# Optimization experiments

Measured on AMD Instinct MI355X. Metric: run time of the kernel, lower is better.

Reference implementation:

```python
import jax, jax.numpy as jnp
import numpy as np

N, D, B = 50000, 256, 2048
SIGMA = 1.0
SIGMA2 = SIGMA * SIGMA  # module stores np.square(sigma)


def setup_inputs() -> dict:
    key = jax.random.key(0)
    k1, k2, k3, k4 = jax.random.split(key, 4)
    x = jax.random.normal(k1, (B, D), dtype=jnp.float32)
    data_set = jax.random.normal(k2, (N, D), dtype=jnp.float32)
    # labels are +/-1
    data_labels = jnp.where(jax.random.uniform(k3, (N,)) < 0.5, -1.0, 1.0).astype(jnp.float32)
    # lambdas initialized to ones in the module; use small positive noise around 1/n scale
    lambdas = jax.random.uniform(k4, (N,), dtype=jnp.float32) * (2.0 / N)
    b = jnp.ones((1,), dtype=jnp.float32)
    return {"x": x, "data_set": data_set, "data_labels": data_labels,
            "lambdas": lambdas, "b": b}


def reference(x, data_set, data_labels, lambdas, b):
    x2 = jnp.sum(x * x, axis=1, keepdims=True)            # [B,1]
    s2 = jnp.sum(data_set * data_set, axis=1)             # [N]
    cross = jnp.einsum('bd,nd->bn', x, data_set)          # [B,N]
    sqdist = x2 + s2[None, :] - 2.0 * cross               # [B,N]
    K = jnp.exp(-sqdist / (2.0 * SIGMA2))                 # rbf kernel [B,N]
    w = data_labels * jax.nn.relu(lambdas)                # [N]
    return jnp.tanh(K @ w + b)                            # [B]
```

## Files before the change

kernel.cpp:

```cpp
#include <hip/hip_runtime.h>
#include <hip/hip_bf16.h>
#include <hip/hip_fp8.h>
#include <math.h>

#define NPTS 50000
#define DIM  256
#define BQ   2048
#define NPAD 50048

#define CH   32
#define NCH32 1564
#define NG   96
#define LOG2E 1.4426950408889634f

#define WS_ACC 0
#define WS_X2  2048
#define WS_T   4096
#define WS_SGN 54144
#define WS_XB  104192
#define WS_SB  366336
#define WS_TOTAL_BYTES (6772480ull * 4ull)

#define V1_ACC 0
#define V1_X2  2048
#define V1_S2  4096
#define V1_W   54096

typedef __bf16 bf16x8 __attribute__((ext_vector_type(8)));
typedef __bf16 bf16x4 __attribute__((ext_vector_type(4)));
typedef float  f32x4  __attribute__((ext_vector_type(4)));
typedef float  f32x16 __attribute__((ext_vector_type(16)));
typedef int    i32x4  __attribute__((ext_vector_type(4)));
typedef int    i32x8  __attribute__((ext_vector_type(8)));
typedef unsigned int u32;
typedef unsigned char u8;

__device__ __forceinline__ float fast_exp2(float v) {
#if __has_builtin(__builtin_amdgcn_exp2f)
  return __builtin_amdgcn_exp2f(v);
#else
  return exp2f(v);
#endif
}

__device__ __forceinline__ float fast_log2(float v) {
#if __has_builtin(__builtin_amdgcn_logf)
  return __builtin_amdgcn_logf(v);
#else
  return __log2f(v);
#endif
}

__device__ __forceinline__ void async_copy16(const void* g, void* l) {
  __builtin_amdgcn_global_load_lds(
      (const __attribute__((address_space(1))) u32*)g,
      (__attribute__((address_space(3))) u32*)l, 16, 0, 0);
}

__device__ __forceinline__ u32 pack_fp8x4(float4 v) {
#if __has_builtin(__builtin_amdgcn_cvt_pk_fp8_f32)
  int pk = __builtin_amdgcn_cvt_pk_fp8_f32(v.x, v.y, 0, false);
  pk = __builtin_amdgcn_cvt_pk_fp8_f32(v.z, v.w, pk, true);
  return (u32)pk;
#else
  __hip_fp8_e4m3 a(v.x), b(v.y), c(v.z), d(v.w);
  return (u32)a.__x | ((u32)b.__x << 8) | ((u32)c.__x << 16) | ((u32)d.__x << 24);
#endif
}


__global__ __launch_bounds__(256) void svm_precvt10(
    const float* __restrict__ x, const float* __restrict__ s,
    const float* __restrict__ labels, const float* __restrict__ lambdas,
    float* __restrict__ ws) {
  const int wid  = blockIdx.x * 4 + (threadIdx.x >> 6);
  const int lane = threadIdx.x & 63;
  u8* xb8 = (u8*)(ws + WS_XB);
  u8* sb8 = (u8*)(ws + WS_SB);

  if (blockIdx.x < 8) ws[WS_ACC + blockIdx.x * 256 + threadIdx.x] = 0.0f;

  if (wid < NPAD) {
    float4 v = make_float4(0.f, 0.f, 0.f, 0.f);
    if (wid < NPTS)
      v = reinterpret_cast<const float4*>(s + (size_t)wid * DIM)[lane];
    ((u32*)(sb8 + (size_t)wid * DIM))[lane] = pack_fp8x4(v);
    float ss = v.x * v.x + v.y * v.y + v.z * v.z + v.w * v.w;
    #pragma unroll
    for (int off = 32; off > 0; off >>= 1) ss += __shfl_xor(ss, off);
    if (lane == 0) {
      float s2h = 0.5f * LOG2E * ss;
      float lam = (wid < NPTS) ? lambdas[wid] : 0.0f;
      float lab = (wid < NPTS) ? labels[wid] : 1.0f;
      float mag = lam > 0.0f ? lam : 0.0f;
      ws[WS_T + wid]   = (mag > 0.0f) ? s2h - fast_log2(mag) : __builtin_inff();
      ws[WS_SGN + wid] = lab;
    }
  } else if (wid < NPAD + BQ) {
    int r = wid - NPAD;
    float4 v = reinterpret_cast<const float4*>(x + (size_t)r * DIM)[lane];
    ((u32*)(xb8 + (size_t)r * DIM))[lane] = pack_fp8x4(v);
    float ss = v.x * v.x + v.y * v.y + v.z * v.z + v.w * v.w;
    #pragma unroll
    for (int off = 32; off > 0; off >>= 1) ss += __shfl_xor(ss, off);
    if (lane == 0) ws[WS_X2 + r] = 0.5f * LOG2E * ss;
  }
}

__global__ __launch_bounds__(256, 2) void svm_main21(float* __restrict__ ws) {
  __shared__ u8 sB[3][8192];

  const u8* xb8 = (const u8*)(ws + WS_XB);
  const u8* sb8 = (const u8*)(ws + WS_SB);
  const float* x2g = ws + WS_X2;
  const float* tg  = ws + WS_T;
  const float* sgg = ws + WS_SGN;
  float* accOut    = ws + WS_ACC;

  const int t    = threadIdx.x;
  const int wave = t >> 6;
  const int lane = t & 63;
  const int l32  = lane & 31;
  const int hk   = lane >> 5;
  const int g    = blockIdx.x % NG;
  const int mt   = blockIdx.x / NG;
  const int m0   = mt * 256;
  const int c0   = (NCH32 * g) / NG;
  const int c1   = (NCH32 * (g + 1)) / NG;

#define STAGE21(buf, cc)                                                      \
  do {                                                                        \
    _Pragma("unroll")                                                         \
    for (int i = 0; i < 2; ++i) {                                             \
      int p  = wave * 2 + i;                                        \
      int kt = p >> 1;                                              \
      int h  = p & 1;                                                         \
      int r  = h * 16 + (lane >> 2);                                          \
      int q  = (lane & 3) ^ ((r >> 1) & 3);                                   \
      const u8* src = sb8 + (size_t)((cc) * CH + r) * DIM + kt * 64 + q * 16; \
      async_copy16(src, &sB[(buf)][kt * 2048 + h * 1024 + lane * 16]);        \
    }                                                                         \
  } while (0)

  STAGE21(0, c0);
  STAGE21(1, c0 + 1);

  i32x8 afr[2][4];
  #pragma unroll
  for (int mi = 0; mi < 2; ++mi)
    #pragma unroll
    for (int kt = 0; kt < 4; ++kt) {
      const u8* ap = xb8 + (size_t)(m0 + wave * 64 + mi * 32 + l32) * DIM
                         + kt * 64 + hk * 32;
      i32x4 a0 = *reinterpret_cast<const i32x4*>(ap);
      i32x4 a1 = *reinterpret_cast<const i32x4*>(ap + 16);
      afr[mi][kt] = __builtin_shufflevector(a0, a1, 0, 1, 2, 3, 4, 5, 6, 7);
    }
  #pragma unroll
  for (int mi = 0; mi < 2; ++mi)
    #pragma unroll
    for (int kt = 0; kt < 4; ++kt)
      asm volatile("" : "+v"(afr[mi][kt]));

  float runAcc0[16], runAcc1[16];
  #pragma unroll
  for (int i = 0; i < 16; ++i) { runAcc0[i] = 0.0f; runAcc1[i] = 0.0f; }

  asm volatile("s_waitcnt vmcnt(2)" ::: "memory");
  __builtin_amdgcn_s_barrier();

  int cur = 0;
  for (int c = c0; c < c1; ++c) {
    float tt = tg[c * CH + l32];
    float sg = sgg[c * CH + l32];
    __builtin_amdgcn_sched_barrier(0);

    {
      int c2 = c + 2;
      if (c2 < c1) {
        int b2 = cur + 2; if (b2 >= 3) b2 -= 3;
        STAGE21(b2, c2);
      }
    }

    f32x16 acc0 = (f32x16)(0.0f), acc1 = (f32x16)(0.0f);
    const u8* bufB = &sB[cur][0];
    __builtin_amdgcn_s_setprio(1);
    #pragma unroll
    for (int kt = 0; kt < 4; ++kt) {
      int s0 = ((l32 << 2) | (hk << 1)) ^ ((l32 >> 1) & 3);
      const u8* bp = bufB + kt * 2048;
      i32x4 lo = *reinterpret_cast<const i32x4*>(bp + s0 * 16);
      i32x4 hi = *reinterpret_cast<const i32x4*>(bp + (s0 ^ 1) * 16);
      i32x8 bfr = __builtin_shufflevector(lo, hi, 0, 1, 2, 3, 4, 5, 6, 7);
      acc0 = __builtin_amdgcn_mfma_scale_f32_32x32x64_f8f6f4(
          afr[0][kt], bfr, acc0, 0, 0, 0, 0x7F7F7F7F, 0, 0x7F7F7F7F);
      acc1 = __builtin_amdgcn_mfma_scale_f32_32x32x64_f8f6f4(
          afr[1][kt], bfr, acc1, 0, 0, 0, 0x7F7F7F7F, 0, 0x7F7F7F7F);
    }
    __builtin_amdgcn_s_setprio(0);

    #pragma unroll
    for (int reg = 0; reg < 16; ++reg)
      runAcc0[reg] = __builtin_fmaf(
          sg, fast_exp2(__builtin_fmaf(acc0[reg], LOG2E, -tt)), runAcc0[reg]);
    #pragma unroll
    for (int reg = 0; reg < 16; ++reg)
      runAcc1[reg] = __builtin_fmaf(
          sg, fast_exp2(__builtin_fmaf(acc1[reg], LOG2E, -tt)), runAcc1[reg]);

    __builtin_amdgcn_s_barrier();
    asm volatile("" ::: "memory");
    cur = (cur + 1 < 3) ? cur + 1 : 0;
  }

  #pragma unroll
  for (int reg = 0; reg < 16; ++reg) {
    float v = runAcc0[reg];
    v += __shfl_xor(v, 1);
    v += __shfl_xor(v, 2);
    v += __shfl_xor(v, 4);
    v += __shfl_xor(v, 8);
    v += __shfl_xor(v, 16);
    if (l32 == 0) {
      int row = m0 + wave * 64 + (reg & 3) + 8 * (reg >> 2) + 4 * hk;
      atomicAdd(&accOut[row], fast_exp2(-x2g[row]) * v);
    }
  }
  #pragma unroll
  for (int reg = 0; reg < 16; ++reg) {
    float v = runAcc1[reg];
    v += __shfl_xor(v, 1);
    v += __shfl_xor(v, 2);
    v += __shfl_xor(v, 4);
    v += __shfl_xor(v, 8);
    v += __shfl_xor(v, 16);
    if (l32 == 0) {
      int row = m0 + wave * 64 + 32 + (reg & 3) + 8 * (reg >> 2) + 4 * hk;
      atomicAdd(&accOut[row], fast_exp2(-x2g[row]) * v);
    }
  }
#undef STAGE21
}


#define BK 32

__global__ __launch_bounds__(256) void svm_precompute(
    const float* __restrict__ x, const float* __restrict__ s,
    const float* __restrict__ labels, const float* __restrict__ lambdas,
    float* __restrict__ ws) {
  int wid  = blockIdx.x * 4 + (threadIdx.x >> 6);
  int lane = threadIdx.x & 63;
  const float* src;
  if (wid < NPTS)           src = s + (size_t)wid * DIM;
  else if (wid < NPTS + BQ) src = x + (size_t)(wid - NPTS) * DIM;
  else return;
  float4 v = reinterpret_cast<const float4*>(src)[lane];
  float ss = v.x * v.x + v.y * v.y + v.z * v.z + v.w * v.w;
  #pragma unroll
  for (int off = 32; off > 0; off >>= 1) ss += __shfl_xor(ss, off);
  if (lane == 0) {
    if (wid < NPTS) {
      ws[V1_S2 + wid] = ss;
      float lam = lambdas[wid];
      ws[V1_W + wid] = labels[wid] * (lam > 0.0f ? lam : 0.0f);
    } else {
      ws[V1_X2 + (wid - NPTS)] = ss;
    }
  }
}

__global__ __launch_bounds__(256) void svm_main(
    const float* __restrict__ x, const float* __restrict__ s,
    const float* __restrict__ ws) {
  __shared__ __bf16 sA[128 * BK];
  __shared__ __bf16 sB2[128 * BK];

  const int t    = threadIdx.x;
  const int wave = t >> 6;
  const int lane = t & 63;
  const int quad = lane >> 4;
  const int l16  = lane & 15;
  const int wm   = (wave & 1) * 64;
  const int wn   = (wave >> 1) * 64;
  const int bRow0 = blockIdx.y * 128;
  const int n0    = blockIdx.x * 128;

  f32x4 acc[4][4];
  #pragma unroll
  for (int i = 0; i < 4; ++i)
    #pragma unroll
    for (int j = 0; j < 4; ++j)
      acc[i][j] = (f32x4)(0.0f);

  for (int kt = 0; kt < DIM / BK; ++kt) {
    const int k0 = kt * BK;
    __syncthreads();
    #pragma unroll
    for (int i = 0; i < 4; ++i) {
      int slot = t + i * 256;
      int r  = slot >> 3;
      int c4 = slot & 7;
      float4 va = reinterpret_cast<const float4*>(
          x + (size_t)(bRow0 + r) * DIM + k0)[c4];
      bf16x4 ha = { (__bf16)va.x, (__bf16)va.y, (__bf16)va.z, (__bf16)va.w };
      *reinterpret_cast<bf16x4*>(&sA[r * BK + c4 * 4]) = ha;

      int nrow = n0 + r;
      float4 vb = make_float4(0.f, 0.f, 0.f, 0.f);
      if (nrow < NPTS)
        vb = reinterpret_cast<const float4*>(
            s + (size_t)nrow * DIM + k0)[c4];
      bf16x4 hb = { (__bf16)vb.x, (__bf16)vb.y, (__bf16)vb.z, (__bf16)vb.w };
      *reinterpret_cast<bf16x4*>(&sB2[r * BK + c4 * 4]) = hb;
    }
    __syncthreads();

    bf16x8 af[4], bfv[4];
    #pragma unroll
    for (int mi = 0; mi < 4; ++mi)
      af[mi] = *reinterpret_cast<const bf16x8*>(
          &sA[(wm + mi * 16 + l16) * BK + quad * 8]);
    #pragma unroll
    for (int ni = 0; ni < 4; ++ni)
      bfv[ni] = *reinterpret_cast<const bf16x8*>(
          &sB2[(wn + ni * 16 + l16) * BK + quad * 8]);
    #pragma unroll
    for (int mi = 0; mi < 4; ++mi)
      #pragma unroll
      for (int ni = 0; ni < 4; ++ni)
        acc[mi][ni] = __builtin_amdgcn_mfma_f32_16x16x32_bf16(
            af[mi], bfv[ni], acc[mi][ni], 0, 0, 0);
  }

  const float* x2g = ws + V1_X2;
  const float* s2g = ws + V1_S2;
  const float* wg  = ws + V1_W;
  float* accOut    = (float*)ws + V1_ACC;

  float s2v[4], wv[4];
  #pragma unroll
  for (int ni = 0; ni < 4; ++ni) {
    int n = n0 + wn + ni * 16 + l16;
    bool ok = n < NPTS;
    s2v[ni] = ok ? s2g[n] : 0.0f;
    wv[ni]  = ok ? wg[n]  : 0.0f;
  }
  #pragma unroll
  for (int mi = 0; mi < 4; ++mi) {
    const int mbase = wm + mi * 16 + quad * 4;
    #pragma unroll
    for (int reg = 0; reg < 4; ++reg) {
      float x2r = x2g[bRow0 + mbase + reg];
      float ps = 0.0f;
      #pragma unroll
      for (int ni = 0; ni < 4; ++ni) {
        float cc = acc[mi][ni][reg];
        ps += __expf(__builtin_fmaf(-0.5f, x2r + s2v[ni], cc)) * wv[ni];
      }
      ps += __shfl_xor(ps, 1);
      ps += __shfl_xor(ps, 2);
      ps += __shfl_xor(ps, 4);
      ps += __shfl_xor(ps, 8);
      if (l16 == 0) atomicAdd(&accOut[bRow0 + mbase + reg], ps);
    }
  }
}


__global__ __launch_bounds__(256) void svm_finalize(
    const float* __restrict__ ws, const float* __restrict__ bias,
    float* __restrict__ out) {
  int i = blockIdx.x * 256 + threadIdx.x;
  if (i < BQ) out[i] = tanhf(ws[i] + bias[0]);
}

extern "C" void kernel_launch(void* const* d_in, const int* in_sizes, int n_in,
                              void* d_out, int out_size, void* d_ws, size_t ws_size,
                              hipStream_t stream) {
  const float* x       = (const float*)d_in[0];
  const float* s       = (const float*)d_in[1];
  const float* labels  = (const float*)d_in[2];
  const float* lambdas = (const float*)d_in[3];
  const float* bias    = (const float*)d_in[4];
  float* out = (float*)d_out;
  float* ws  = (float*)d_ws;

  if (ws_size >= WS_TOTAL_BYTES) {
    svm_precvt10<<<(NPAD + BQ + 3) / 4, 256, 0, stream>>>(x, s, labels, lambdas, ws);
    svm_main21<<<8 * NG, 256, 0, stream>>>(ws);
  } else {
    hipMemsetAsync(ws, 0, BQ * sizeof(float), stream);
    svm_precompute<<<(NPTS + BQ + 3) / 4, 256, 0, stream>>>(x, s, labels, lambdas, ws);
    dim3 grid(391, BQ / 128);
    svm_main<<<grid, 256, 0, stream>>>(x, s, ws);
  }
  svm_finalize<<<BQ / 256, 256, 0, stream>>>(ws, bias, out);
}
```

Before: 156.3 us.

## Widen N-chunk to 64, cut grid to 512 blocks, fuse finalize via last-block tanh

```diff
diff --git a/kernel.cpp b/kernel.cpp
--- a/kernel.cpp
+++ b/kernel.cpp
@@ -8,9 +8,9 @@
 #define BQ   2048
 #define NPAD 50048
 
-#define CH   32
-#define NCH32 1564
-#define NG   96
+#define CH   64
+#define NCH64 782
+#define NG   64
 #define LOG2E 1.4426950408889634f
 
 #define WS_ACC 0
@@ -18,6 +18,7 @@
 #define WS_T   4096
 #define WS_SGN 54144
 #define WS_XB  104192
+#define WS_CNT 235264
 #define WS_SB  366336
 #define WS_TOTAL_BYTES (6772480ull * 4ull)
 
@@ -79,6 +80,7 @@
   u8* sb8 = (u8*)(ws + WS_SB);
 
   if (blockIdx.x < 8) ws[WS_ACC + blockIdx.x * 256 + threadIdx.x] = 0.0f;
+  if (blockIdx.x == 8 && threadIdx.x == 0) *(u32*)(ws + WS_CNT) = 0u;
 
   if (wid < NPAD) {
     float4 v = make_float4(0.f, 0.f, 0.f, 0.f);
@@ -107,8 +109,11 @@
   }
 }
 
-__global__ __launch_bounds__(256, 2) void svm_main21(float* __restrict__ ws) {
-  __shared__ u8 sB[3][8192];
+__global__ __launch_bounds__(256, 2) void svm_main22(
+    float* __restrict__ ws, const float* __restrict__ bias,
+    float* __restrict__ out) {
+  __shared__ u8 sB[3][16384];
+  __shared__ bool isLast;
 
   const u8* xb8 = (const u8*)(ws + WS_XB);
   const u8* sb8 = (const u8*)(ws + WS_SB);
@@ -122,28 +127,28 @@
   const int lane = t & 63;
   const int l32  = lane & 31;
   const int hk   = lane >> 5;
-  const int g    = blockIdx.x % NG;
-  const int mt   = blockIdx.x / NG;
+  const int g    = blockIdx.x & (NG - 1);
+  const int mt   = blockIdx.x >> 6;
   const int m0   = mt * 256;
-  const int c0   = (NCH32 * g) / NG;
-  const int c1   = (NCH32 * (g + 1)) / NG;
-
-#define STAGE21(buf, cc)                                                      \
+  const int c0   = (NCH64 * g) / NG;
+  const int c1   = (NCH64 * (g + 1)) / NG;
+
+#define STAGE22(buf, cc)                                                      \
   do {                                                                        \
     _Pragma("unroll")                                                         \
-    for (int i = 0; i < 2; ++i) {                                             \
-      int p  = wave * 2 + i;                                        \
-      int kt = p >> 1;                                              \
-      int h  = p & 1;                                                         \
-      int r  = h * 16 + (lane >> 2);                                          \
+    for (int i = 0; i < 4; ++i) {                                             \
+      int p  = wave * 4 + i;                                       \
+      int kt = p >> 2;                                             \
+      int h  = p & 3;                                                         \
+      int r  = h * 16 + (lane >> 2);                               \
       int q  = (lane & 3) ^ ((r >> 1) & 3);                                   \
       const u8* src = sb8 + (size_t)((cc) * CH + r) * DIM + kt * 64 + q * 16; \
-      async_copy16(src, &sB[(buf)][kt * 2048 + h * 1024 + lane * 16]);        \
+      async_copy16(src, &sB[(buf)][kt * 4096 + h * 1024 + lane * 16]);        \
     }                                                                         \
   } while (0)
 
-  STAGE21(0, c0);
-  STAGE21(1, c0 + 1);
+  STAGE22(0, c0);
+  STAGE22(1, c0 + 1);
 
   i32x8 afr[2][4];
   #pragma unroll
@@ -166,48 +171,66 @@
   #pragma unroll
   for (int i = 0; i < 16; ++i) { runAcc0[i] = 0.0f; runAcc1[i] = 0.0f; }
 
-  asm volatile("s_waitcnt vmcnt(2)" ::: "memory");
+  asm volatile("s_waitcnt vmcnt(4)" ::: "memory");
   __builtin_amdgcn_s_barrier();
 
   int cur = 0;
   for (int c = c0; c < c1; ++c) {
-    float tt = tg[c * CH + l32];
-    float sg = sgg[c * CH + l32];
+    float tt0 = tg[c * CH + l32];
+    float sg0 = sgg[c * CH + l32];
+    float tt1 = tg[c * CH + 32 + l32];
+    float sg1 = sgg[c * CH + 32 + l32];
     __builtin_amdgcn_sched_barrier(0);
 
     {
       int c2 = c + 2;
       if (c2 < c1) {
         int b2 = cur + 2; if (b2 >= 3) b2 -= 3;
-        STAGE21(b2, c2);
+        STAGE22(b2, c2);
       }
     }
 
-    f32x16 acc0 = (f32x16)(0.0f), acc1 = (f32x16)(0.0f);
+    f32x16 acc00 = (f32x16)(0.0f), acc01 = (f32x16)(0.0f);
+    f32x16 acc10 = (f32x16)(0.0f), acc11 = (f32x16)(0.0f);
     const u8* bufB = &sB[cur][0];
-    __builtin_amdgcn_s_setprio(1);
     #pragma unroll
     for (int kt = 0; kt < 4; ++kt) {
-      int s0 = ((l32 << 2) | (hk << 1)) ^ ((l32 >> 1) & 3);
-      const u8* bp = bufB + kt * 2048;
-      i32x4 lo = *reinterpret_cast<const i32x4*>(bp + s0 * 16);
-      i32x4 hi = *reinterpret_cast<const i32x4*>(bp + (s0 ^ 1) * 16);
-      i32x8 bfr = __builtin_shufflevector(lo, hi, 0, 1, 2, 3, 4, 5, 6, 7);
-      acc0 = __builtin_amdgcn_mfma_scale_f32_32x32x64_f8f6f4(
-          afr[0][kt], bfr, acc0, 0, 0, 0, 0x7F7F7F7F, 0, 0x7F7F7F7F);
-      acc1 = __builtin_amdgcn_mfma_scale_f32_32x32x64_f8f6f4(
-          afr[1][kt], bfr, acc1, 0, 0, 0, 0x7F7F7F7F, 0, 0x7F7F7F7F);
-    }
-    __builtin_amdgcn_s_setprio(0);
-
-    #pragma unroll
-    for (int reg = 0; reg < 16; ++reg)
-      runAcc0[reg] = __builtin_fmaf(
-          sg, fast_exp2(__builtin_fmaf(acc0[reg], LOG2E, -tt)), runAcc0[reg]);
-    #pragma unroll
-    for (int reg = 0; reg < 16; ++reg)
-      runAcc1[reg] = __builtin_fmaf(
-          sg, fast_exp2(__builtin_fmaf(acc1[reg], LOG2E, -tt)), runAcc1[reg]);
+      const u8* bp = bufB + kt * 4096;
+      int r0 = l32;
+      int s0 = ((r0 << 2) | (hk << 1)) ^ ((r0 >> 1) & 3);
+      i32x4 lo0 = *reinterpret_cast<const i32x4*>(bp + s0 * 16);
+      i32x4 hi0 = *reinterpret_cast<const i32x4*>(bp + (s0 ^ 1) * 16);
+      i32x8 bfr0 = __builtin_shufflevector(lo0, hi0, 0, 1, 2, 3, 4, 5, 6, 7);
+      int r1 = 32 + l32;
+      int s1 = ((r1 << 2) | (hk << 1)) ^ ((r1 >> 1) & 3);
+      i32x4 lo1 = *reinterpret_cast<const i32x4*>(bp + s1 * 16);
+      i32x4 hi1 = *reinterpret_cast<const i32x4*>(bp + (s1 ^ 1) * 16);
+      i32x8 bfr1 = __builtin_shufflevector(lo1, hi1, 0, 1, 2, 3, 4, 5, 6, 7);
+      acc00 = __builtin_amdgcn_mfma_scale_f32_32x32x64_f8f6f4(
+          afr[0][kt], bfr0, acc00, 0, 0, 0, 0x7F7F7F7F, 0, 0x7F7F7F7F);
+      acc01 = __builtin_amdgcn_mfma_scale_f32_32x32x64_f8f6f4(
+          afr[0][kt], bfr1, acc01, 0, 0, 0, 0x7F7F7F7F, 0, 0x7F7F7F7F);
+      acc10 = __builtin_amdgcn_mfma_scale_f32_32x32x64_f8f6f4(
+          afr[1][kt], bfr0, acc10, 0, 0, 0, 0x7F7F7F7F, 0, 0x7F7F7F7F);
+      acc11 = __builtin_amdgcn_mfma_scale_f32_32x32x64_f8f6f4(
+          afr[1][kt], bfr1, acc11, 0, 0, 0, 0x7F7F7F7F, 0, 0x7F7F7F7F);
+    }
+
+    #pragma unroll
+    for (int reg = 0; reg < 16; ++reg) {
+      float p0 = runAcc0[reg];
+      p0 = __builtin_fmaf(
+          sg0, fast_exp2(__builtin_fmaf(acc00[reg], LOG2E, -tt0)), p0);
+      p0 = __builtin_fmaf(
+          sg1, fast_exp2(__builtin_fmaf(acc01[reg], LOG2E, -tt1)), p0);
+      runAcc0[reg] = p0;
+      float p1 = runAcc1[reg];
+      p1 = __builtin_fmaf(
+          sg0, fast_exp2(__builtin_fmaf(acc10[reg], LOG2E, -tt0)), p1);
+      p1 = __builtin_fmaf(
+          sg1, fast_exp2(__builtin_fmaf(acc11[reg], LOG2E, -tt1)), p1);
+      runAcc1[reg] = p1;
+    }
 
     __builtin_amdgcn_s_barrier();
     asm volatile("" ::: "memory");
@@ -240,7 +263,22 @@
       atomicAdd(&accOut[row], fast_exp2(-x2g[row]) * v);
     }
   }
-#undef STAGE21
+
+  __threadfence();
+  __syncthreads();
+  if (threadIdx.x == 0) {
+    u32 old = atomicAdd((u32*)(ws + WS_CNT), 1u);
+    isLast = (old == (u32)(gridDim.x - 1));
+  }
+  __syncthreads();
+  if (isLast) {
+    __threadfence();
+    for (int i = threadIdx.x; i < BQ; i += 256) {
+      float v = atomicAdd(&accOut[i], 0.0f);
+      out[i] = tanhf(v + bias[0]);
+    }
+  }
+#undef STAGE22
 }
 
 
@@ -389,12 +427,12 @@
 
   if (ws_size >= WS_TOTAL_BYTES) {
     svm_precvt10<<<(NPAD + BQ + 3) / 4, 256, 0, stream>>>(x, s, labels, lambdas, ws);
-    svm_main21<<<8 * NG, 256, 0, stream>>>(ws);
+    svm_main22<<<8 * NG, 256, 0, stream>>>(ws, bias, out);
   } else {
     hipMemsetAsync(ws, 0, BQ * sizeof(float), stream);
     svm_precompute<<<(NPTS + BQ + 3) / 4, 256, 0, stream>>>(x, s, labels, lambdas, ws);
     dim3 grid(391, BQ / 128);
     svm_main<<<grid, 256, 0, stream>>>(x, s, ws);
-  }
-  svm_finalize<<<BQ / 256, 256, 0, stream>>>(ws, bias, out);
-}
+    svm_finalize<<<BQ / 256, 256, 0, stream>>>(ws, bias, out);
+  }
+}
```

Result: slower. 175.1 us (+12.0%).
